# Kernel tuning notes

Measured on AMD Instinct MI355X. Metric: run time of the kernel, lower is better.

## Reference

```python
import jax, jax.numpy as jnp
import numpy as np

B, C, H, W = 4, 256, 64, 64
C8 = C // 8


def setup_inputs() -> dict:
    key = jax.random.key(0)
    ks = jax.random.split(key, 8)
    s = 1.0 / np.sqrt(C)
    return {
        "x_ccd": jax.random.normal(ks[0], (B, C, H, W), jnp.float32),
        "x_dem": jax.random.normal(ks[1], (B, C, H, W), jnp.float32),
        "Wq": jax.random.normal(ks[2], (C8, C), jnp.float32) * s,
        "bq": jax.random.normal(ks[3], (C8,), jnp.float32) * 0.01,
        "Wk": jax.random.normal(ks[4], (C8, C), jnp.float32) * s,
        "bk": jax.random.normal(ks[5], (C8,), jnp.float32) * 0.01,
        "Wv": jax.random.normal(ks[6], (C, C), jnp.float32) * s,
        "bv": jax.random.normal(ks[7], (C,), jnp.float32) * 0.01,
        "gamma": jnp.zeros((1,), jnp.float32),
    }


def reference(x_ccd, x_dem, Wq, bq, Wk, bk, Wv, bv, gamma):
    b, c, h, w = x_ccd.shape
    n = h * w
    xc = x_ccd.reshape(b, c, n)  # [B,C,N]
    xd = x_dem.reshape(b, c, n)
    # 1x1 convs == per-pixel linear projections
    q = jnp.einsum("oc,bcn->bno", Wq, xc) + bq  # [B,N,C8]
    k = jnp.einsum("oc,bcn->bon", Wk, xd) + bk[None, :, None]  # [B,C8,N]
    energy = jnp.einsum("bno,bom->bnm", q, k)  # [B,N,N]
    attention = jax.nn.softmax(energy, axis=-1)
    v = jnp.einsum("oc,bcn->bon", Wv, xd) + bv[None, :, None]  # [B,C,N]
    out = jnp.einsum("bom,bnm->bon", v, attention)  # value @ attention^T
    out = out.reshape(b, c, h, w)
    return gamma * out + x_ccd
```

## Files before the change

### kernel.cpp

```cpp
#include <hip/hip_runtime.h>

typedef unsigned short u16;
typedef unsigned int u32;
typedef short v8s __attribute__((ext_vector_type(8)));
typedef float v16f __attribute__((ext_vector_type(16)));

#define MFMA(a, b, c) __builtin_amdgcn_mfma_f32_32x32x16_bf16(a, b, c, 0, 0, 0)
#define L2E 1.44269504088896f

union U8 { v8s s; uint4 u4; u32 u[4]; };

__device__ __forceinline__ u16 f2bf(float x) {
    u32 u = __float_as_uint(x);
    return (u16)((u + 0x7FFFu + ((u >> 16) & 1u)) >> 16);
}
__device__ __forceinline__ u32 pk2(float a, float b) {
    return (u32)f2bf(a) | ((u32)f2bf(b) << 16);
}
__device__ __forceinline__ u32 pkz(float e0, float e1) {
    return __builtin_amdgcn_perm(__float_as_uint(e1), __float_as_uint(e0), 0x07060302u);
}


__global__ __launch_bounds__(256) void prep_w_kernel(
    const float* __restrict__ Wq, const float* __restrict__ bq,
    const float* __restrict__ Wk, const float* __restrict__ bk,
    const float* __restrict__ Wv, const float* __restrict__ bv,
    u16* __restrict__ WfT, float* __restrict__ ball)
{
    int tid = blockIdx.x * 256 + threadIdx.x;
    if (tid < 81920) {
        int ch = tid >> 8, c = tid & 255;
        float w;
        if (ch < 32)      w = Wq[ch * 256 + c];
        else if (ch < 64) w = Wk[(ch - 32) * 256 + c] * L2E;
        else              w = Wv[(ch - 64) * 256 + c];
        int tile = (ch >> 5) * 16 + (c >> 4);
        int lane = ((c >> 3) & 1) * 32 + (ch & 31);
        WfT[tile * 512 + lane * 8 + (c & 7)] = f2bf(w);
    } else if (tid < 82240) {
        int i = tid - 81920;
        float bb;
        if (i < 32)      bb = bq[i];
        else if (i < 64) bb = bk[i - 32] * L2E;
        else             bb = bv[i - 64];
        ball[i] = bb;
    }
}

__global__ __launch_bounds__(256) void transpose_kernel(
    const float* __restrict__ xc, const float* __restrict__ xd,
    u16* __restrict__ xcfT, u16* __restrict__ xdfT)
{
    __shared__ float tile[64][65];
    int blk = blockIdx.x;
    int arr = blk >> 10, rem = blk & 1023;
    int b = rem >> 8, rem2 = rem & 255;
    int c0 = (rem2 >> 6) * 64, n0 = (rem2 & 63) * 64;
    const float* src = arr ? xd : xc;
    u16* dst = arr ? xdfT : xcfT;
    int t = threadIdx.x;
#pragma unroll
    for (int p = 0; p < 4; p++) {
        int idx = p * 256 + t;
        int c = idx >> 4, n4 = (idx & 15) * 4;
        float4 v = *(const float4*)&src[((size_t)(b * 256 + c0 + c)) * 4096 + n0 + n4];
        tile[c][n4] = v.x; tile[c][n4 + 1] = v.y; tile[c][n4 + 2] = v.z; tile[c][n4 + 3] = v.w;
    }
    __syncthreads();
#pragma unroll
    for (int p = 0; p < 2; p++) {
        int idx = p * 256 + t;
        int n = idx >> 3, c8 = (idx & 7) * 8;
        float e[8];
#pragma unroll
        for (int j = 0; j < 8; j++) e[j] = tile[c8 + j][n];
        int ng = n0 + n, cg = c0 + c8;
        size_t off = (((size_t)(b * 128 + (ng >> 5)) * 16 + (cg >> 4)) * 512)
                   + (((cg >> 3) & 1) * 32 + (ng & 31)) * 8;
        uint4 st = make_uint4(pk2(e[0], e[1]), pk2(e[2], e[3]), pk2(e[4], e[5]), pk2(e[6], e[7]));
        *(uint4*)&dst[off] = st;
    }
}

__global__ __launch_bounds__(256) void proj_mfma_kernel(
    const u16* __restrict__ xcfT, const u16* __restrict__ xdfT,
    const u16* __restrict__ WfT, const float* __restrict__ ball,
    u16* __restrict__ qfT, u16* __restrict__ kfT, u16* __restrict__ vfT)
{
    int blk = blockIdx.x, b = blk >> 6, n0g = (blk & 63) * 64;
    int t = threadIdx.x, lane = t & 63, wv = t >> 6;
    int hl = lane >> 5, l31 = lane & 31;
    int nh = wv >> 1, isk = wv & 1;
    int n = n0g + nh * 32 + l31;
    int nt = (n0g >> 5) + nh;

    const u16* xcb = xcfT + ((size_t)(b * 128 + nt) * 16) * 512 + lane * 8;
    const u16* xdb = xdfT + ((size_t)(b * 128 + nt) * 16) * 512 + lane * 8;
    const u16* wqk = WfT + (size_t)(isk * 16) * 512 + lane * 8;
    const u16* wvb = WfT + (size_t)((2 + isk * 4) * 16) * 512 + lane * 8;

    v16f aqk = {};
    v16f av[4] = {};
#pragma unroll
    for (int kc = 0; kc < 16; kc++) {
        U8 bxc, bxd, a;
        bxc.u4 = *(const uint4*)(xcb + kc * 512);
        bxd.u4 = *(const uint4*)(xdb + kc * 512);
        a.u4 = *(const uint4*)(wqk + kc * 512);
        aqk = MFMA(a.s, isk ? bxd.s : bxc.s, aqk);
#pragma unroll
        for (int i = 0; i < 4; i++) {
            U8 aw;
            aw.u4 = *(const uint4*)(wvb + (i * 16 + kc) * 512);
            av[i] = MFMA(aw.s, bxd.s, av[i]);
        }
    }
    u16* qkdst = isk ? kfT : qfT;
#pragma unroll
    for (int i = 0; i < 8; i++) {
        int r = 2 * i;
        int row = (r & 3) + 8 * (r >> 2) + 4 * hl;
        float b0 = ball[isk * 32 + row], b1 = ball[isk * 32 + row + 1];
        u32 st = pk2(aqk[r] + b0, aqk[r + 1] + b1);
        size_t off = (((size_t)(b * 128 + nt) * 2 + (row >> 4)) * 512)
                   + (((row >> 3) & 1) * 32 + l31) * 8 + (row & 7);
        *(u32*)&qkdst[off] = st;
    }
    int vl = ((n >> 3) & 1) * 32;
    int tk = n >> 4, j = n & 7;
#pragma unroll
    for (int i = 0; i < 4; i++) {
        int ct = isk * 4 + i;
        int chb = isk * 128 + i * 32;
        u16* vdst = vfT + (((size_t)(b * 8 + ct) * 256 + tk) * 512) + vl * 8 + j;
#pragma unroll
        for (int r = 0; r < 16; r++) {
            int row = (r & 3) + 8 * (r >> 2) + 4 * hl;
            vdst[row * 8] = f2bf(av[i][r] + ball[64 + chb + row]);
        }
    }
}

__global__ __launch_bounds__(256, 2) void flash_kernel(
    const u16* __restrict__ qfT, const u16* __restrict__ kfT,
    const u16* __restrict__ vfT, const float* __restrict__ xccd,
    const float* __restrict__ gptr, float* __restrict__ outp)
{
    __shared__ float red[2][4][16][64];
    __shared__ float lred[32];

    const int t = threadIdx.x, lane = t & 63, wv = t >> 6;
    const int hl = lane >> 5, l31 = lane & 31;
    const int blk = blockIdx.x;
    const int b = (blk & 7) >> 1;
    const int qt = ((blk >> 3) << 1) | (blk & 1);
    const int n0 = qt * 32;
    const int kh = wv & 1, chh = wv >> 1;
    const int chbase = chh * 128;

    U8 qf0, qf1;
    {
        const u16* qp = qfT + ((size_t)(b * 128 + (n0 >> 5)) * 2) * 512 + lane * 8;
        qf0.u4 = *(const uint4*)qp;
        qf1.u4 = *(const uint4*)(qp + 512);
    }
    U8 ones;
#pragma unroll
    for (int i = 0; i < 8; i++) ones.s[i] = (short)0x3F80;

    v16f acc[4] = {};
    v16f lac = {};

    const u16* kbase = kfT + ((size_t)b * 128 * 2) * 512 + lane * 8;
    const u16* vbase = vfT + ((size_t)(b * 8 + chh * 4) * 256) * 512 + lane * 8;

    U8 kA[2], kB[2], vA[4][2], vB[4][2];

    auto load_frags = [&](int it, U8 (&kf)[2], U8 (&vf)[4][2]) {
        const int kt = it * 2 + kh;
        kf[0].u4 = *(const uint4*)(kbase + (size_t)(kt * 2) * 512);
        kf[1].u4 = *(const uint4*)(kbase + (size_t)(kt * 2 + 1) * 512);
        const int tk = it * 4 + kh * 2;
#pragma unroll
        for (int ct = 0; ct < 4; ct++) {
            const u16* vp = vbase + ((size_t)(ct * 256 + tk)) * 512;
            vf[ct][0].u4 = *(const uint4*)vp;
            vf[ct][1].u4 = *(const uint4*)(vp + 512);
        }
    };

    load_frags(0, kA, vA);

    auto step = [&](int it, U8 (&kf)[2], U8 (&vf)[4][2], U8 (&kn)[2], U8 (&vn)[4][2]) {
        if (it < 63) load_frags(it + 1, kn, vn);
        v16f E = {};
        E = MFMA(kf[0].s, qf0.s, E);
        E = MFMA(kf[1].s, qf1.s, E);
        u32 pkv[8];
#pragma unroll
        for (int j = 0; j < 8; j++)
            pkv[j] = pkz(exp2f(E[2 * j]), exp2f(E[2 * j + 1]));
#pragma unroll
        for (int kc = 0; kc < 2; kc++) {
            const int pb = kc * 4;
            u32 p01 = pkv[pb], p23 = pkv[pb + 1];
            u32 p45 = pkv[pb + 2], p67 = pkv[pb + 3];
            u32 s0 = hl ? p01 : p45;
            u32 s1 = hl ? p23 : p67;
            u32 r0 = (u32)__shfl_xor((int)s0, 32, 64);
            u32 r1 = (u32)__shfl_xor((int)s1, 32, 64);
            U8 B;
            B.u[0] = hl ? r0 : p01;
            B.u[1] = hl ? r1 : p23;
            B.u[2] = hl ? p45 : r0;
            B.u[3] = hl ? p67 : r1;
            lac = MFMA(ones.s, B.s, lac);
#pragma unroll
            for (int ct = 0; ct < 4; ct++)
                acc[ct] = MFMA(vf[ct][kc].s, B.s, acc[ct]);
        }
    };
#pragma unroll 1
    for (int it = 0; it < 64; it += 2) {
        step(it, kA, vA, kB, vB);
        step(it + 1, kB, vB, kA, vA);
    }
    if (kh == 1) {
#pragma unroll
        for (int ct = 0; ct < 4; ct++)
#pragma unroll
            for (int r = 0; r < 16; r++)
                red[chh][ct][r][lane] = acc[ct][r];
        if (chh == 0 && lane < 32) lred[l31] = lac[0];
    }
    __syncthreads();
    if (kh == 0) {
        const float g = gptr[0];
        const float sc = g / (lac[0] + lred[l31]);
#pragma unroll
        for (int ct = 0; ct < 4; ct++)
#pragma unroll
            for (int r = 0; r < 16; r++) {
                float v = acc[ct][r] + red[chh][ct][r][lane];
                int ch = chbase + ct * 32 + (r & 3) + 8 * (r >> 2) + 4 * hl;
                size_t ga = ((size_t)(b * 256 + ch)) * 4096 + n0 + l31;
                outp[ga] = v * sc + xccd[ga];
            }
    }
}

extern "C" void kernel_launch(void* const* d_in, const int* in_sizes, int n_in,
                              void* d_out, int out_size, void* d_ws, size_t ws_size,
                              hipStream_t stream)
{
    const float* xc    = (const float*)d_in[0];
    const float* xd    = (const float*)d_in[1];
    const float* Wq    = (const float*)d_in[2];
    const float* bq    = (const float*)d_in[3];
    const float* Wk    = (const float*)d_in[4];
    const float* bk    = (const float*)d_in[5];
    const float* Wv    = (const float*)d_in[6];
    const float* bv    = (const float*)d_in[7];
    const float* gamma = (const float*)d_in[8];
    float* out = (float*)d_out;

    u16* qfT  = (u16*)d_ws;
    u16* kfT  = qfT + (size_t)524288;
    u16* vfT  = kfT + (size_t)524288;
    u16* xcfT = vfT + (size_t)4194304;
    u16* xdfT = xcfT + (size_t)4194304;
    u16* WfT  = xdfT + (size_t)4194304;
    float* bl = (float*)(WfT + 81920);

    prep_w_kernel<<<322, 256, 0, stream>>>(Wq, bq, Wk, bk, Wv, bv, WfT, bl);
    transpose_kernel<<<2048, 256, 0, stream>>>(xc, xd, xcfT, xdfT);
    proj_mfma_kernel<<<256, 256, 0, stream>>>(xcfT, xdfT, WfT, bl, qfT, kfT, vfT);
    flash_kernel<<<512, 256, 0, stream>>>(qfT, kfT, vfT, xc, gamma, out);
}
```

Measured before the change: 182.0 us.

## Fuse transpose into projection via LDS staging; widen flash blocks to two query tiles

Drops the separate transpose kernel and its bf16 global intermediates. The projection kernel now loads fp32 x tiles directly, converts them to bf16 and transposes them into double-buffered LDS. The flash kernel moves to 512-thread blocks that cover two 32-query tiles, halving the grid, with an extra query-half index in the reduction buffers. This saves a launch and global round trip, but the LDS transposed stores may hit bank conflicts, and the larger flash blocks change occupancy while reusing K/V only within a block.

```diff
diff --git a/kernel.cpp b/kernel.cpp
--- a/kernel.cpp
+++ b/kernel.cpp
@@ -48,73 +48,67 @@
     }
 }
 
-__global__ __launch_bounds__(256) void transpose_kernel(
+__global__ __launch_bounds__(256) void proj_fused_kernel(
     const float* __restrict__ xc, const float* __restrict__ xd,
-    u16* __restrict__ xcfT, u16* __restrict__ xdfT)
-{
-    __shared__ float tile[64][65];
-    int blk = blockIdx.x;
-    int arr = blk >> 10, rem = blk & 1023;
-    int b = rem >> 8, rem2 = rem & 255;
-    int c0 = (rem2 >> 6) * 64, n0 = (rem2 & 63) * 64;
-    const float* src = arr ? xd : xc;
-    u16* dst = arr ? xdfT : xcfT;
-    int t = threadIdx.x;
-#pragma unroll
-    for (int p = 0; p < 4; p++) {
-        int idx = p * 256 + t;
-        int c = idx >> 4, n4 = (idx & 15) * 4;
-        float4 v = *(const float4*)&src[((size_t)(b * 256 + c0 + c)) * 4096 + n0 + n4];
-        tile[c][n4] = v.x; tile[c][n4 + 1] = v.y; tile[c][n4 + 2] = v.z; tile[c][n4 + 3] = v.w;
-    }
-    __syncthreads();
-#pragma unroll
-    for (int p = 0; p < 2; p++) {
-        int idx = p * 256 + t;
-        int n = idx >> 3, c8 = (idx & 7) * 8;
-        float e[8];
-#pragma unroll
-        for (int j = 0; j < 8; j++) e[j] = tile[c8 + j][n];
-        int ng = n0 + n, cg = c0 + c8;
-        size_t off = (((size_t)(b * 128 + (ng >> 5)) * 16 + (cg >> 4)) * 512)
-                   + (((cg >> 3) & 1) * 32 + (ng & 31)) * 8;
-        uint4 st = make_uint4(pk2(e[0], e[1]), pk2(e[2], e[3]), pk2(e[4], e[5]), pk2(e[6], e[7]));
-        *(uint4*)&dst[off] = st;
-    }
-}
-
-__global__ __launch_bounds__(256) void proj_mfma_kernel(
-    const u16* __restrict__ xcfT, const u16* __restrict__ xdfT,
     const u16* __restrict__ WfT, const float* __restrict__ ball,
     u16* __restrict__ qfT, u16* __restrict__ kfT, u16* __restrict__ vfT)
 {
-    int blk = blockIdx.x, b = blk >> 6, n0g = (blk & 63) * 64;
+    __shared__ u16 xls[2][2][64][72];
+    int blk = blockIdx.x, b = blk >> 6, n0 = (blk & 63) * 64;
     int t = threadIdx.x, lane = t & 63, wv = t >> 6;
     int hl = lane >> 5, l31 = lane & 31;
     int nh = wv >> 1, isk = wv & 1;
-    int n = n0g + nh * 32 + l31;
-    int nt = (n0g >> 5) + nh;
-
-    const u16* xcb = xcfT + ((size_t)(b * 128 + nt) * 16) * 512 + lane * 8;
-    const u16* xdb = xdfT + ((size_t)(b * 128 + nt) * 16) * 512 + lane * 8;
+    int n = n0 + nh * 32 + l31;
+    int nt = (n0 >> 5) + nh;
+
+    auto stage = [&](int cc, int bf) {
+#pragma unroll
+        for (int it2 = 0; it2 < 4; it2++) {
+            int slot = it2 * 256 + t;
+            int c = slot >> 4, n4 = (slot & 15) * 4;
+            size_t gofs = ((size_t)(b * 256 + cc * 64 + c)) * 4096 + n0 + n4;
+            float4 vc = *(const float4*)&xc[gofs];
+            float4 vd = *(const float4*)&xd[gofs];
+            xls[bf][0][n4 + 0][c] = f2bf(vc.x);
+            xls[bf][0][n4 + 1][c] = f2bf(vc.y);
+            xls[bf][0][n4 + 2][c] = f2bf(vc.z);
+            xls[bf][0][n4 + 3][c] = f2bf(vc.w);
+            xls[bf][1][n4 + 0][c] = f2bf(vd.x);
+            xls[bf][1][n4 + 1][c] = f2bf(vd.y);
+            xls[bf][1][n4 + 2][c] = f2bf(vd.z);
+            xls[bf][1][n4 + 3][c] = f2bf(vd.w);
+        }
+    };
+
     const u16* wqk = WfT + (size_t)(isk * 16) * 512 + lane * 8;
     const u16* wvb = WfT + (size_t)((2 + isk * 4) * 16) * 512 + lane * 8;
+    int nrow = nh * 32 + l31;
 
     v16f aqk = {};
     v16f av[4] = {};
-#pragma unroll
-    for (int kc = 0; kc < 16; kc++) {
-        U8 bxc, bxd, a;
-        bxc.u4 = *(const uint4*)(xcb + kc * 512);
-        bxd.u4 = *(const uint4*)(xdb + kc * 512);
-        a.u4 = *(const uint4*)(wqk + kc * 512);
-        aqk = MFMA(a.s, isk ? bxd.s : bxc.s, aqk);
-#pragma unroll
-        for (int i = 0; i < 4; i++) {
-            U8 aw;
-            aw.u4 = *(const uint4*)(wvb + (i * 16 + kc) * 512);
-            av[i] = MFMA(aw.s, bxd.s, av[i]);
-        }
+
+    stage(0, 0);
+    __syncthreads();
+#pragma unroll 1
+    for (int cc = 0; cc < 4; cc++) {
+        if (cc < 3) stage(cc + 1, (cc + 1) & 1);
+        int bf = cc & 1;
+#pragma unroll
+        for (int kcL = 0; kcL < 4; kcL++) {
+            int kc = cc * 4 + kcL;
+            U8 bxc, bxd, a;
+            bxc.u4 = *(const uint4*)&xls[bf][0][nrow][kcL * 16 + hl * 8];
+            bxd.u4 = *(const uint4*)&xls[bf][1][nrow][kcL * 16 + hl * 8];
+            a.u4 = *(const uint4*)(wqk + (size_t)kc * 512);
+            aqk = MFMA(a.s, isk ? bxd.s : bxc.s, aqk);
+#pragma unroll
+            for (int i = 0; i < 4; i++) {
+                U8 aw;
+                aw.u4 = *(const uint4*)(wvb + (size_t)(i * 16 + kc) * 512);
+                av[i] = MFMA(aw.s, bxd.s, av[i]);
+            }
+        }
+        __syncthreads();
     }
     u16* qkdst = isk ? kfT : qfT;
 #pragma unroll
@@ -142,21 +136,21 @@
     }
 }
 
-__global__ __launch_bounds__(256, 2) void flash_kernel(
+__global__ __launch_bounds__(512, 2) void flash_kernel(
     const u16* __restrict__ qfT, const u16* __restrict__ kfT,
     const u16* __restrict__ vfT, const float* __restrict__ xccd,
     const float* __restrict__ gptr, float* __restrict__ outp)
 {
-    __shared__ float red[2][4][16][64];
-    __shared__ float lred[32];
+    __shared__ float red[2][2][4][16][64];
+    __shared__ float lred[2][32];
 
     const int t = threadIdx.x, lane = t & 63, wv = t >> 6;
     const int hl = lane >> 5, l31 = lane & 31;
     const int blk = blockIdx.x;
     const int b = (blk & 7) >> 1;
     const int qt = ((blk >> 3) << 1) | (blk & 1);
-    const int n0 = qt * 32;
-    const int kh = wv & 1, chh = wv >> 1;
+    const int kh = wv & 1, chh = (wv >> 1) & 1, qh = wv >> 2;
+    const int n0 = qt * 64 + qh * 32;
     const int chbase = chh * 128;
 
     U8 qf0, qf1;
@@ -231,18 +225,18 @@
         for (int ct = 0; ct < 4; ct++)
 #pragma unroll
             for (int r = 0; r < 16; r++)
-                red[chh][ct][r][lane] = acc[ct][r];
-        if (chh == 0 && lane < 32) lred[l31] = lac[0];
+                red[qh][chh][ct][r][lane] = acc[ct][r];
+        if (chh == 0 && lane < 32) lred[qh][l31] = lac[0];
     }
     __syncthreads();
     if (kh == 0) {
         const float g = gptr[0];
-        const float sc = g / (lac[0] + lred[l31]);
+        const float sc = g / (lac[0] + lred[qh][l31]);
 #pragma unroll
         for (int ct = 0; ct < 4; ct++)
 #pragma unroll
             for (int r = 0; r < 16; r++) {
-                float v = acc[ct][r] + red[chh][ct][r][lane];
+                float v = acc[ct][r] + red[qh][chh][ct][r][lane];
                 int ch = chbase + ct * 32 + (r & 3) + 8 * (r >> 2) + 4 * hl;
                 size_t ga = ((size_t)(b * 256 + ch)) * 4096 + n0 + l31;
                 outp[ga] = v * sc + xccd[ga];
@@ -268,13 +262,10 @@
     u16* qfT  = (u16*)d_ws;
     u16* kfT  = qfT + (size_t)524288;
     u16* vfT  = kfT + (size_t)524288;
-    u16* xcfT = vfT + (size_t)4194304;
-    u16* xdfT = xcfT + (size_t)4194304;
-    u16* WfT  = xdfT + (size_t)4194304;
+    u16* WfT  = vfT + (size_t)4194304;
     float* bl = (float*)(WfT + 81920);
 
     prep_w_kernel<<<322, 256, 0, stream>>>(Wq, bq, Wk, bk, Wv, bv, WfT, bl);
-    transpose_kernel<<<2048, 256, 0, stream>>>(xc, xd, xcfT, xdfT);
-    proj_mfma_kernel<<<256, 256, 0, stream>>>(xcfT, xdfT, WfT, bl, qfT, kfT, vfT);
-    flash_kernel<<<512, 256, 0, stream>>>(qfT, kfT, vfT, xc, gamma, out);
-}
+    proj_fused_kernel<<<256, 256, 0, stream>>>(xc, xd, WfT, bl, qfT, kfT, vfT);
+    flash_kernel<<<256, 512, 0, stream>>>(qfT, kfT, vfT, xc, gamma, out);
+}
```

Result: faster. 174.9 us (-3.9%).
